# Kernel tuning notes

Hardware: AMD Instinct MI355X
Metric: run time of the kernel (lower is better)

The kernel has to match this reference:

```python
import jax, jax.numpy as jnp
import numpy as np

RADIUS = 4
SIGMA_X = 4.0
SIGMA_I = 10.0
P = 64                      # patch_size
NS = 2 * RADIUS + 1         # neighborhood_size = 9
EPS = float(np.finfo(np.float64).eps)


def _dist_weights():
    # Faithful to torch: dist varies only along the LAST window axis
    # (torch `expand` of a 1-D tensor to (9,9,9) broadcasts along dim -1).
    d = jnp.arange(1, NS + 1) - (RADIUS + 1)          # -4..4
    dist3d = jnp.broadcast_to(3 * d ** 2, (NS, NS, NS)).astype(jnp.float32)
    mask = (dist3d <= RADIUS).astype(jnp.float32)
    return (mask * jnp.exp(-dist3d / SIGMA_X ** 2)).reshape(-1)  # (729,)


_OFFSETS = jnp.asarray(
    np.stack(np.meshgrid(np.arange(NS), np.arange(NS), np.arange(NS), indexing='ij'),
             axis=-1).reshape(-1, 3), dtype=jnp.int32)            # (729, 3)


def _forward(batch, preds):
    B = batch.shape[0]
    K = preds.shape[1]
    pad = [(0, 0), (0, 0), (RADIUS, RADIUS), (RADIUS, RADIUS), (RADIUS, RADIUS)]
    pb = jnp.pad(batch, pad, constant_values=EPS)   # [B,1,P+2r,P+2r,P+2r]
    pp = jnp.pad(preds, pad, constant_values=EPS)   # [B,K,P+2r,P+2r,P+2r]
    dw = _dist_weights()

    def body(carry, od):
        off, w_o = od
        num, den = carry
        img_win = jax.lax.dynamic_slice(pb, (0, 0, off[0], off[1], off[2]),
                                        (B, 1, P, P, P))
        # Gaussian intensity affinity * spatial weight for this offset
        w = jnp.exp(-(img_win - batch) ** 2 / SIGMA_I ** 2) * w_o   # [B,1,P,P,P]
        pred_win = jax.lax.dynamic_slice(pp, (0, 0, off[0], off[1], off[2]),
                                         (B, K, P, P, P))
        return (num + w * pred_win, den + w), None

    num0 = jnp.zeros((B, K, P, P, P), batch.dtype)
    den0 = jnp.zeros((B, 1, P, P, P), batch.dtype)
    (num_map, den_map), _ = jax.lax.scan(body, (num0, den0), (_OFFSETS, dw))

    # Faithful to torch broadcasting: preds[B,1,P,P,P] * map[B,P,P,P] -> [B,B,...],
    # i.e. each sample's preds are contracted with the batch-summed maps.
    num_s = num_map.sum(axis=0)          # [K,P,P,P]
    den_s = den_map.sum(axis=0)[0]       # [P,P,P]
    numerator = jnp.einsum('bkxyz,kxyz->bk', preds, num_s)
    denominator = jnp.einsum('bkxyz,xyz->bk', preds, den_s)
    loss = (numerator + EPS) / (denominator + EPS)   # [B,K]
    return K - loss.sum(axis=1)                      # [B]


def setup_inputs() -> dict:
    key = jax.random.key(0)
    k1, k2 = jax.random.split(key)
    batch = jax.random.uniform(k1, (4, 1, P, P, P), dtype=jnp.float32)
    preds = jax.random.uniform(k2, (4, 4, P, P, P), dtype=jnp.float32)
    return {"batch": batch, "preds": preds}


def reference(batch, preds):
    return _forward(batch, preds)
```

## Files before the change

### kernel.cpp

```cpp
#include <hip/hip_runtime.h>


constexpr int Pdim = 64;
constexpr int P3   = Pdim * Pdim * Pdim;
constexpr int NREP = 16;

#define EPSF 2.2204460492503131e-16f

constexpr float WZ1   = 0.8290291181804004f;
constexpr float K2F   = 0.014426950408889634f;
constexpr float C1F   = 0.02f;
constexpr float WFULL = 81.0f * (1.0f + 2.0f * WZ1);

template<int X0, int NX, int FIRSTW>
__device__ __forceinline__ void passx_body(const float* __restrict__ Ip,
                                           const float* __restrict__ Pp,
                                           float* __restrict__ U0,
                                           float* __restrict__ U1,
                                           bool isden) {
  float w0[9], w1[9];
#pragma unroll
  for (int i = 0; i < 9; ++i) { w0[i] = 0.f; w1[i] = 0.f; }
  float s0 = 0.f, s1 = 0.f;
#pragma unroll
  for (int i = 0; i < NX; ++i) {
    const int x = X0 + i;
    float u0 = 0.f, u1 = 0.f;
    if (x < 64) {
      float I = Ip[x << 12];
      float g = exp2f(-I * I * K2F);
      float p = isden ? 1.f : Pp[x << 12];
      u0 = g * p;
      u1 = u0 * I;
    }
    const int r = i % 9;
    s0 += u0 - w0[r]; w0[r] = u0;
    s1 += u1 - w1[r]; w1[r] = u1;
    if (i >= FIRSTW) {
      U0[(x - 4) << 12] = s0;
      U1[(x - 4) << 12] = s1;
    }
  }
}

__global__ __launch_bounds__(256)
void ncuts_passx(const float* __restrict__ batch, const float* __restrict__ preds,
                 float* __restrict__ U, float* __restrict__ acc) {
  const int t = threadIdx.x;
  if (blockIdx.x == 0 && blockIdx.y == 0 && blockIdx.z == 0) {
    acc[t] = 0.f; acc[t + 256] = 0.f;
  }
  const int z  = t & 63, ys = t >> 6;
  const int y  = blockIdx.x * 4 + ys;
  const int pair = blockIdx.y;
  const int b = pair / 5, c = pair - 5 * b;
  const bool isden = (c == 4);
  const int lin = (y << 6) + z;
  const float* Ip = batch + b * P3 + lin;
  const float* Pp = isden ? Ip : preds + (b * 4 + c) * P3 + lin;
  float* U0 = U + (pair * 2 + 0) * P3 + lin;
  float* U1 = U + (pair * 2 + 1) * P3 + lin;
  if (blockIdx.z == 0) passx_body< 0, 36, 4>(Ip, Pp, U0, U1, isden);
  else                 passx_body<28, 40, 8>(Ip, Pp, U0, U1, isden);
}

__global__ __launch_bounds__(256)
void ncuts_passy(float* __restrict__ U) {
  const int t = threadIdx.x;
  const int z = t & 63, xs = t >> 6;
  const int x = blockIdx.x * 4 + xs;
  const int fi = blockIdx.y;
  float* base = U + fi * P3 + (x << 12) + z;
  float w[9];
#pragma unroll
  for (int i = 0; i < 9; ++i) w[i] = 0.f;
  float s = 0.f;
#pragma unroll
  for (int y = 0; y < 68; ++y) {
    float u = (y < 64) ? base[y << 6] : 0.f;
    const int r = y % 9;
    s += u - w[r]; w[r] = u;
    if (y >= 4) base[(y - 4) << 6] = s;
  }
}

__global__ __launch_bounds__(256)
void ncuts_contract(const float* __restrict__ batch, const float* __restrict__ preds,
                    const float* __restrict__ U, float* __restrict__ acc) {
  __shared__ float red[4][32];
  const int t = threadIdx.x;
  float pn[16], pd[16];
#pragma unroll
  for (int i = 0; i < 16; ++i) { pn[i] = 0.f; pd[i] = 0.f; }

#pragma unroll 1
  for (int it = 0; it < 2; ++it) {
    const int v = blockIdx.x * 512 + it * 256 + t;
    const int z = v & 63, y = (v >> 6) & 63, x = v >> 12;

    float a0[4], a1[4], gsum = 0.f;
#pragma unroll
    for (int b = 0; b < 4; ++b) {
      float I = batch[b * P3 + v];
      float g = exp2f(-I * I * K2F);
      a0[b] = g; a1[b] = g * I * C1F; gsum += g;
    }

    const bool zm = (z > 0), zp = (z < 63);
    float ns[4] = {0.f, 0.f, 0.f, 0.f};
    float ds = 0.f;
#pragma unroll
    for (int b = 0; b < 4; ++b) {
#pragma unroll
      for (int c = 0; c < 5; ++c) {
        const float* up = U + ((b * 5 + c) * 2) * P3 + v;
#pragma unroll
        for (int m = 0; m < 2; ++m) {
          const float* u = up + m * P3;
          float um = u[-1]; um = zm ? um : 0.f;
          float uc = u[0];
          float uq = u[1];  uq = zp ? uq : 0.f;
          float Zc = __builtin_fmaf(WZ1, um + uq, uc);
          float a = m ? a1[b] : a0[b];
          if (c < 4) ns[c] = __builtin_fmaf(a, Zc, ns[c]);
          else       ds    = __builtin_fmaf(a, Zc, ds);
        }
      }
    }
    float cx = (float)(9 - max(0, 4 - x) - max(0, x - 59));
    float cy = (float)(9 - max(0, 4 - y) - max(0, y - 59));
    float cz = 1.f + WZ1 * (float)((int)zm + (int)zp);
    ds = __builtin_fmaf(gsum, WFULL - cx * cy * cz, ds);

#pragma unroll
    for (int b = 0; b < 4; ++b) {
#pragma unroll
      for (int k = 0; k < 4; ++k) {
        float p = preds[(b * 4 + k) * P3 + v];
        pn[b * 4 + k] = __builtin_fmaf(p, ns[k], pn[b * 4 + k]);
        pd[b * 4 + k] = __builtin_fmaf(p, ds,    pd[b * 4 + k]);
      }
    }
  }

#pragma unroll
  for (int i = 0; i < 16; ++i) {
#pragma unroll
    for (int off = 32; off > 0; off >>= 1) {
      pn[i] += __shfl_down(pn[i], off, 64);
      pd[i] += __shfl_down(pd[i], off, 64);
    }
  }
  const int wave = t >> 6, lane = t & 63;
  if (lane == 0) {
#pragma unroll
    for (int i = 0; i < 16; ++i) { red[wave][i] = pn[i]; red[wave][16 + i] = pd[i]; }
  }
  __syncthreads();
  if (t < 32) {
    float s = red[0][t] + red[1][t] + red[2][t] + red[3][t];
    atomicAdd(&acc[(blockIdx.x & (NREP - 1)) * 32 + t], s);
  }
}

__global__ void ncuts_final(const float* __restrict__ acc, float* __restrict__ out) {
  __shared__ float loss[16];
  int t = threadIdx.x;
  if (t < 16) {
    float n = 0.f, d = 0.f;
    for (int r = 0; r < NREP; ++r) { n += acc[r * 32 + t]; d += acc[r * 32 + 16 + t]; }
    loss[t] = (n + EPSF) / (d + EPSF);
  }
  __syncthreads();
  if (t < 4) {
    float s = loss[t * 4] + loss[t * 4 + 1] + loss[t * 4 + 2] + loss[t * 4 + 3];
    out[t] = 4.0f - s;
  }
}

constexpr int Rxy = 4;
constexpr int TX = 8, TY = 8;
constexpr int ZLEN = 2;
constexpr int RGX = 16, RGY = 16, RGZ = 10;
constexpr int YP = 17, ZP = 11;

__global__ __launch_bounds__(256, 2)
void ncuts_main(const float* __restrict__ batch, const float* __restrict__ preds,
                float* __restrict__ acc) {
  __shared__ float  sB[RGX][YP][ZP];
  __shared__ float4 sP[RGX][YP][ZP];
  __shared__ float  red[4][32];

  const int t = threadIdx.x;
  const int tx = t & 7, ty = (t >> 3) & 7, tzt = t >> 6;
  const int bx0 = blockIdx.x * TX, by0 = blockIdx.y * TY, bz0 = blockIdx.z * 8;
  const int x = bx0 + tx, y = by0 + ty, z0 = bz0 + tzt * ZLEN;
  const int zc = tzt * ZLEN;

  float  den[ZLEN];
  float4 num[ZLEN];
#pragma unroll
  for (int j = 0; j < ZLEN; ++j) { den[j] = 0.f; num[j] = make_float4(0.f, 0.f, 0.f, 0.f); }

  const float C1 = -0.014426950408889634f;
  const float LWZ1 = -0.27050531991668065f;

  for (int b = 0; b < 4; ++b) {
    __syncthreads();
    for (int idx = t; idx < RGX * RGY * RGZ; idx += 256) {
      int rz = idx % RGZ, rq = idx / RGZ, ry = rq % RGY, rx = rq / RGY;
      int gx = bx0 + rx - Rxy, gy = by0 + ry - Rxy, gz = bz0 + rz - 1;
      bool in = ((unsigned)gx < 64u) & ((unsigned)gy < 64u) & ((unsigned)gz < 64u);
      float v = EPSF; float4 pv = make_float4(EPSF, EPSF, EPSF, EPSF);
      if (in) {
        int gi = (gx * Pdim + gy) * Pdim + gz;
        v = batch[b * P3 + gi];
        const float* pp = preds + b * 4 * P3 + gi;
        pv.x = pp[0]; pv.y = pp[P3]; pv.z = pp[2 * P3]; pv.w = pp[3 * P3];
      }
      sB[rx][ry][rz] = v; sP[rx][ry][rz] = pv;
    }
    __syncthreads();

    float I0[ZLEN];
#pragma unroll
    for (int j = 0; j < ZLEN; ++j) I0[j] = sB[tx + Rxy][ty + Rxy][zc + 1 + j];

#pragma unroll 1
    for (int dy = 0; dy < 9; ++dy) {
#pragma unroll 3
      for (int dx = 0; dx < 9; ++dx) {
        const float*  cb = &sB[tx + dx][ty + dy][zc];
        const float4* cp = &sP[tx + dx][ty + dy][zc];
        float colB[ZLEN + 2]; float4 colP[ZLEN + 2];
#pragma unroll
        for (int j = 0; j < ZLEN + 2; ++j) { colB[j] = cb[j]; colP[j] = cp[j]; }
#pragma unroll
        for (int j = 0; j < ZLEN; ++j) {
#pragma unroll
          for (int dz = 0; dz < 3; ++dz) {
            float d = colB[j + dz] - I0[j];
            float arg = __builtin_fmaf(d * d, C1, (dz == 1) ? 0.f : LWZ1);
            float w = exp2f(arg);
            den[j] += w;
            float4 p = colP[j + dz];
            num[j].x = __builtin_fmaf(w, p.x, num[j].x);
            num[j].y = __builtin_fmaf(w, p.y, num[j].y);
            num[j].z = __builtin_fmaf(w, p.z, num[j].z);
            num[j].w = __builtin_fmaf(w, p.w, num[j].w);
          }
        }
      }
    }
  }

  float pn[16], pd[16];
#pragma unroll
  for (int i = 0; i < 16; ++i) { pn[i] = 0.f; pd[i] = 0.f; }
#pragma unroll
  for (int b = 0; b < 4; ++b) {
#pragma unroll
    for (int j = 0; j < ZLEN; ++j) {
      const float* pp = preds + b * 4 * P3 + ((x * Pdim + y) * Pdim + z0 + j);
      float nsv[4] = {num[j].x, num[j].y, num[j].z, num[j].w};
#pragma unroll
      for (int k = 0; k < 4; ++k) {
        float pv = pp[k * P3];
        pn[b * 4 + k] = __builtin_fmaf(pv, nsv[k], pn[b * 4 + k]);
        pd[b * 4 + k] = __builtin_fmaf(pv, den[j], pd[b * 4 + k]);
      }
    }
  }
#pragma unroll
  for (int i = 0; i < 16; ++i) {
#pragma unroll
    for (int off = 32; off > 0; off >>= 1) {
      pn[i] += __shfl_down(pn[i], off, 64);
      pd[i] += __shfl_down(pd[i], off, 64);
    }
  }
  const int wave = t >> 6, lane = t & 63;
  if (lane == 0) {
#pragma unroll
    for (int i = 0; i < 16; ++i) { red[wave][i] = pn[i]; red[wave][16 + i] = pd[i]; }
  }
  __syncthreads();
  if (t < 32) {
    float s = red[0][t] + red[1][t] + red[2][t] + red[3][t];
    int bid = blockIdx.x + 8 * (blockIdx.y + 8 * (int)blockIdx.z);
    atomicAdd(&acc[(bid & (NREP - 1)) * 32 + t], s);
  }
}

__global__ void ncuts_zero(float* __restrict__ acc) {
  int t = threadIdx.x;
  if (t < NREP * 32) acc[t] = 0.f;
}

extern "C" void kernel_launch(void* const* d_in, const int* in_sizes, int n_in,
                              void* d_out, int out_size, void* d_ws, size_t ws_size,
                              hipStream_t stream) {
  const float* batch = (const float*)d_in[0];
  const float* preds = (const float*)d_in[1];
  float* out = (float*)d_out;

  const size_t ubytes = (size_t)40 * P3 * 4;
  const size_t need   = ubytes + 4096;
  if (ws_size >= need) {
    float* U   = (float*)((char*)d_ws + 256);
    float* acc = (float*)((char*)d_ws + ubytes + 1024);
    hipLaunchKernelGGL(ncuts_passx, dim3(16, 20, 2), dim3(256), 0, stream,
                       batch, preds, U, acc);
    hipLaunchKernelGGL(ncuts_passy, dim3(16, 40), dim3(256), 0, stream, U);
    hipLaunchKernelGGL(ncuts_contract, dim3(512), dim3(256), 0, stream,
                       batch, preds, U, acc);
    hipLaunchKernelGGL(ncuts_final, dim3(1), dim3(64), 0, stream, acc, out);
  } else {
    float* acc = (float*)d_ws;
    hipLaunchKernelGGL(ncuts_zero, dim3(1), dim3(512), 0, stream, acc);
    hipLaunchKernelGGL(ncuts_main, dim3(8, 8, 8), dim3(256), 0, stream,
                       batch, preds, acc);
    hipLaunchKernelGGL(ncuts_final, dim3(1), dim3(64), 0, stream, acc, out);
  }
}
```

Baseline: 111.6 us.

## Store separable box-filter intermediates as half2 and fold z-stencil into y pass

The x-pass intermediates are now packed into __half2 pairs instead of two float planes, which halves workspace traffic. The y pass writes to a separate buffer instead of working in place, is split in two along y for more parallelism, and applies the z-direction 3-tap stencil through wavefront shuffles. The contract kernel then reads one half2 per (b,c) instead of six floats. This cuts memory traffic and load count, but fp16 storage of sums up to about 81 loses precision and may hurt accuracy.

```diff
diff --git a/kernel.cpp b/kernel.cpp
--- a/kernel.cpp
+++ b/kernel.cpp
@@ -1,4 +1,5 @@
 #include <hip/hip_runtime.h>
+#include <hip/hip_fp16.h>
 
 
 constexpr int Pdim = 64;
@@ -15,8 +16,7 @@
 template<int X0, int NX, int FIRSTW>
 __device__ __forceinline__ void passx_body(const float* __restrict__ Ip,
                                            const float* __restrict__ Pp,
-                                           float* __restrict__ U0,
-                                           float* __restrict__ U1,
+                                           __half2* __restrict__ Uo,
                                            bool isden) {
   float w0[9], w1[9];
 #pragma unroll
@@ -36,57 +36,75 @@
     const int r = i % 9;
     s0 += u0 - w0[r]; w0[r] = u0;
     s1 += u1 - w1[r]; w1[r] = u1;
-    if (i >= FIRSTW) {
-      U0[(x - 4) << 12] = s0;
-      U1[(x - 4) << 12] = s1;
-    }
+    if (i >= FIRSTW) Uo[(x - 4) << 12] = __floats2half2_rn(s0, s1);
   }
 }
 
 __global__ __launch_bounds__(256)
 void ncuts_passx(const float* __restrict__ batch, const float* __restrict__ preds,
-                 float* __restrict__ U, float* __restrict__ acc) {
+                 __half2* __restrict__ U, float* __restrict__ acc) {
   const int t = threadIdx.x;
   if (blockIdx.x == 0 && blockIdx.y == 0 && blockIdx.z == 0) {
     acc[t] = 0.f; acc[t + 256] = 0.f;
   }
-  const int z  = t & 63, ys = t >> 6;
-  const int y  = blockIdx.x * 4 + ys;
+  const int z = t & 63, ys = t >> 6;
+  const int y = blockIdx.x * 4 + ys;
   const int pair = blockIdx.y;
   const int b = pair / 5, c = pair - 5 * b;
   const bool isden = (c == 4);
   const int lin = (y << 6) + z;
   const float* Ip = batch + b * P3 + lin;
   const float* Pp = isden ? Ip : preds + (b * 4 + c) * P3 + lin;
-  float* U0 = U + (pair * 2 + 0) * P3 + lin;
-  float* U1 = U + (pair * 2 + 1) * P3 + lin;
-  if (blockIdx.z == 0) passx_body< 0, 36, 4>(Ip, Pp, U0, U1, isden);
-  else                 passx_body<28, 40, 8>(Ip, Pp, U0, U1, isden);
+  __half2* Uo = U + pair * P3 + lin;
+  if (blockIdx.z == 0) passx_body< 0, 36, 4>(Ip, Pp, Uo, isden);
+  else                 passx_body<28, 40, 8>(Ip, Pp, Uo, isden);
+}
+
+template<int Y0, int NY, int FIRSTW>
+__device__ __forceinline__ void passyz_body(const __half2* __restrict__ src,
+                                            __half2* __restrict__ dst, int z) {
+  float w0[9], w1[9];
+#pragma unroll
+  for (int i = 0; i < 9; ++i) { w0[i] = 0.f; w1[i] = 0.f; }
+  float s0 = 0.f, s1 = 0.f;
+#pragma unroll
+  for (int i = 0; i < NY; ++i) {
+    const int y = Y0 + i;
+    float u0 = 0.f, u1 = 0.f;
+    if (y < 64) {
+      float2 u = __half22float2(src[y << 6]);
+      u0 = u.x; u1 = u.y;
+    }
+    const int r = i % 9;
+    s0 += u0 - w0[r]; w0[r] = u0;
+    s1 += u1 - w1[r]; w1[r] = u1;
+    if (i >= FIRSTW) {
+      float up0 = __shfl_up(s0, 1, 64),   up1 = __shfl_up(s1, 1, 64);
+      float dn0 = __shfl_down(s0, 1, 64), dn1 = __shfl_down(s1, 1, 64);
+      if (z == 0)  { up0 = 0.f; up1 = 0.f; }
+      if (z == 63) { dn0 = 0.f; dn1 = 0.f; }
+      float v0 = __builtin_fmaf(WZ1, up0 + dn0, s0);
+      float v1 = __builtin_fmaf(WZ1, up1 + dn1, s1);
+      dst[(y - 4) << 6] = __floats2half2_rn(v0, v1);
+    }
+  }
 }
 
 __global__ __launch_bounds__(256)
-void ncuts_passy(float* __restrict__ U) {
+void ncuts_passyz(const __half2* __restrict__ U, __half2* __restrict__ V) {
   const int t = threadIdx.x;
   const int z = t & 63, xs = t >> 6;
   const int x = blockIdx.x * 4 + xs;
-  const int fi = blockIdx.y;
-  float* base = U + fi * P3 + (x << 12) + z;
-  float w[9];
-#pragma unroll
-  for (int i = 0; i < 9; ++i) w[i] = 0.f;
-  float s = 0.f;
-#pragma unroll
-  for (int y = 0; y < 68; ++y) {
-    float u = (y < 64) ? base[y << 6] : 0.f;
-    const int r = y % 9;
-    s += u - w[r]; w[r] = u;
-    if (y >= 4) base[(y - 4) << 6] = s;
-  }
+  const int pair = blockIdx.y;
+  const __half2* src = U + pair * P3 + (x << 12) + z;
+  __half2* dst = V + pair * P3 + (x << 12) + z;
+  if (blockIdx.z == 0) passyz_body< 0, 36, 4>(src, dst, z);
+  else                 passyz_body<28, 40, 8>(src, dst, z);
 }
 
 __global__ __launch_bounds__(256)
 void ncuts_contract(const float* __restrict__ batch, const float* __restrict__ preds,
-                    const float* __restrict__ U, float* __restrict__ acc) {
+                    const __half2* __restrict__ V, float* __restrict__ acc) {
   __shared__ float red[4][32];
   const int t = threadIdx.x;
   float pn[16], pd[16];
@@ -106,30 +124,21 @@
       a0[b] = g; a1[b] = g * I * C1F; gsum += g;
     }
 
-    const bool zm = (z > 0), zp = (z < 63);
     float ns[4] = {0.f, 0.f, 0.f, 0.f};
     float ds = 0.f;
 #pragma unroll
     for (int b = 0; b < 4; ++b) {
 #pragma unroll
       for (int c = 0; c < 5; ++c) {
-        const float* up = U + ((b * 5 + c) * 2) * P3 + v;
-#pragma unroll
-        for (int m = 0; m < 2; ++m) {
-          const float* u = up + m * P3;
-          float um = u[-1]; um = zm ? um : 0.f;
-          float uc = u[0];
-          float uq = u[1];  uq = zp ? uq : 0.f;
-          float Zc = __builtin_fmaf(WZ1, um + uq, uc);
-          float a = m ? a1[b] : a0[b];
-          if (c < 4) ns[c] = __builtin_fmaf(a, Zc, ns[c]);
-          else       ds    = __builtin_fmaf(a, Zc, ds);
-        }
+        float2 u = __half22float2(V[(b * 5 + c) * P3 + v]);
+        float zc = __builtin_fmaf(a0[b], u.x, a1[b] * u.y);
+        if (c < 4) ns[c] += zc;
+        else       ds    += zc;
       }
     }
     float cx = (float)(9 - max(0, 4 - x) - max(0, x - 59));
     float cy = (float)(9 - max(0, 4 - y) - max(0, y - 59));
-    float cz = 1.f + WZ1 * (float)((int)zm + (int)zp);
+    float cz = 1.f + WZ1 * (float)((int)(z > 0) + (int)(z < 63));
     ds = __builtin_fmaf(gsum, WFULL - cx * cy * cz, ds);
 
 #pragma unroll
@@ -304,16 +313,17 @@
   const float* preds = (const float*)d_in[1];
   float* out = (float*)d_out;
 
-  const size_t ubytes = (size_t)40 * P3 * 4;
-  const size_t need   = ubytes + 4096;
+  const size_t fbytes = (size_t)20 * P3 * sizeof(__half2);
+  const size_t need   = 2 * fbytes + 8192;
   if (ws_size >= need) {
-    float* U   = (float*)((char*)d_ws + 256);
-    float* acc = (float*)((char*)d_ws + ubytes + 1024);
-    hipLaunchKernelGGL(ncuts_passx, dim3(16, 20, 2), dim3(256), 0, stream,
+    __half2* U   = (__half2*)((char*)d_ws + 256);
+    __half2* V   = (__half2*)((char*)d_ws + 256 + fbytes);
+    float*   acc = (float*)((char*)d_ws + 512 + 2 * fbytes);
+    hipLaunchKernelGGL(ncuts_passx,  dim3(16, 20, 2), dim3(256), 0, stream,
                        batch, preds, U, acc);
-    hipLaunchKernelGGL(ncuts_passy, dim3(16, 40), dim3(256), 0, stream, U);
+    hipLaunchKernelGGL(ncuts_passyz, dim3(16, 20, 2), dim3(256), 0, stream, U, V);
     hipLaunchKernelGGL(ncuts_contract, dim3(512), dim3(256), 0, stream,
-                       batch, preds, U, acc);
+                       batch, preds, V, acc);
     hipLaunchKernelGGL(ncuts_final, dim3(1), dim3(64), 0, stream, acc, out);
   } else {
     float* acc = (float*)d_ws;
```

Result: faster. 97.08 us (-13.0%).
